# Kernel optimization log

Measured on AMD Instinct MI355X. Metric: run time of the kernel, lower is better.

Reference implementation:

```python
import jax, jax.numpy as jnp
import numpy as np

BN_EPS = 1e-5


def conv(x, w, b=None, stride=1, pad=1):
    out = jax.lax.conv_general_dilated(
        x, w, (stride, stride), [(pad, pad), (pad, pad)],
        dimension_numbers=("NCHW", "OIHW", "NCHW"))
    if b is not None:
        out = out + b[None, :, None, None]
    return out


def bn_relu(x):
    # BatchNorm2d(affine=False) in training mode: per-channel batch stats
    mean = jnp.mean(x, axis=(0, 2, 3), keepdims=True)
    var = jnp.var(x, axis=(0, 2, 3), keepdims=True)
    return jax.nn.relu((x - mean) * jax.lax.rsqrt(var + BN_EPS))


def deform_conv(x, offset, w, b, stride, pad=1):
    # torchvision DeformConv2d semantics, 3x3 kernel, dilation=1
    B, C, H, W = x.shape
    O = w.shape[0]
    K = 9
    Ho, Wo = offset.shape[2], offset.shape[3]
    off = offset.reshape(B, K, 2, Ho, Wo)  # (dy, dx) per kernel tap
    ky, kx = jnp.meshgrid(jnp.arange(3), jnp.arange(3), indexing="ij")
    ky = ky.reshape(K).astype(x.dtype)
    kx = kx.reshape(K).astype(x.dtype)
    oy = (jnp.arange(Ho) * stride - pad).astype(x.dtype)
    ox = (jnp.arange(Wo) * stride - pad).astype(x.dtype)
    # sampling coords [B,K,Ho,Wo]
    ys = oy[None, None, :, None] + ky[None, :, None, None] + off[:, :, 0]
    xs = ox[None, None, None, :] + kx[None, :, None, None] + off[:, :, 1]
    y0 = jnp.floor(ys)
    x0 = jnp.floor(xs)
    wy1 = ys - y0
    wx1 = xs - x0
    imf = x.reshape(B, C, H * W)

    def gather(iy, ix):
        valid = (iy >= 0) & (iy <= H - 1) & (ix >= 0) & (ix <= W - 1)
        iyc = jnp.clip(iy, 0, H - 1).astype(jnp.int32)
        ixc = jnp.clip(ix, 0, W - 1).astype(jnp.int32)
        lin = iyc * W + ixc  # [B,K,Ho,Wo]
        g = jax.vmap(lambda im, li: im[:, li])(imf, lin)  # [B,C,K,Ho,Wo]
        return g * valid[:, None].astype(x.dtype)

    sampled = (gather(y0, x0) * ((1 - wy1) * (1 - wx1))[:, None]
               + gather(y0, x0 + 1) * ((1 - wy1) * wx1)[:, None]
               + gather(y0 + 1, x0) * (wy1 * (1 - wx1))[:, None]
               + gather(y0 + 1, x0 + 1) * (wy1 * wx1)[:, None])
    out = jnp.einsum("ock,bckhw->bohw", w.reshape(O, C, K), sampled)
    return out + b[None, :, None, None]


def avgpool4(x):
    B, C, H, W = x.shape
    return x.reshape(B, C, H // 4, 4, W // 4, 4).mean(axis=(3, 5))


def setup_inputs() -> dict:
    key = jax.random.key(0)
    ks = jax.random.split(key, 20)
    n = jax.random.normal
    s = 0.05
    return {
        "x": n(ks[0], (8, 3, 640, 640), jnp.float32),
        "w_off1": n(ks[1], (18, 3, 3, 3), jnp.float32) * s,
        "b_off1": jnp.zeros((18,), jnp.float32),
        "w_d1": n(ks[2], (64, 3, 3, 3), jnp.float32) * s,
        "b_d1": jnp.zeros((64,), jnp.float32),
        "w_skip": n(ks[3], (64, 3, 1, 1), jnp.float32) * s,
        "b_skip": jnp.zeros((64,), jnp.float32),
        "w_bl1": n(ks[4], (64, 64, 3, 3), jnp.float32) * s,
        "w_bl2": n(ks[5], (64, 64, 3, 3), jnp.float32) * s,
        "w_off2": n(ks[6], (18, 64, 3, 3), jnp.float32) * s,
        "b_off2": jnp.zeros((18,), jnp.float32),
        "w_d2": n(ks[7], (64, 64, 3, 3), jnp.float32) * s,
        "b_d2": jnp.zeros((64,), jnp.float32),
        "w_off3": n(ks[8], (18, 64, 3, 3), jnp.float32) * s,
        "b_off3": jnp.zeros((18,), jnp.float32),
        "w_d3": n(ks[9], (256, 64, 3, 3), jnp.float32) * s,
        "b_d3": jnp.zeros((256,), jnp.float32),
    }


def reference(x, w_off1, b_off1, w_d1, b_d1, w_skip, b_skip, w_bl1, w_bl2,
              w_off2, b_off2, w_d2, b_d2, w_off3, b_off3, w_d3, b_d3):
    offset1 = conv(x, w_off1, b_off1, stride=4)
    d1 = deform_conv(x, offset1, w_d1, b_d1, stride=4)
    skip = conv(avgpool4(x), w_skip, b_skip, stride=1, pad=0)
    f = bn_relu(conv(d1 + skip, w_bl1))
    feat_1_4 = bn_relu(conv(f, w_bl2))
    offset2 = conv(feat_1_4, w_off2, b_off2, stride=2)
    feat_1_8 = deform_conv(feat_1_4, offset2, w_d2, b_d2, stride=2)
    offset3 = conv(feat_1_8, w_off3, b_off3, stride=2)
    feat_1_16 = deform_conv(feat_1_8, offset3, w_d3, b_d3, stride=2)
    return (feat_1_4, feat_1_8, feat_1_16)
```

## Files before the change

kernel.cpp:

```cpp
#include <hip/hip_runtime.h>
#include <hip/hip_bf16.h>
#include <math.h>

#define TPB 256

typedef __attribute__((ext_vector_type(8))) short bf16x8_t;
typedef __attribute__((ext_vector_type(4))) float f32x4_t;
typedef __attribute__((ext_vector_type(4))) int i32x4_t;
typedef __attribute__((ext_vector_type(4))) unsigned short u16x4_t;

static __device__ __forceinline__ float bf16_to_f(unsigned short s) {
    union { unsigned u; float f; } cv;
    cv.u = ((unsigned)s) << 16;
    return cv.f;
}
static __device__ __forceinline__ short f_to_bf16(float v) {
    __hip_bfloat16 h = __float2bfloat16(v);
    return *(short*)&h;
}

__global__ void repack_frag_kernel(const float* __restrict__ w,
                                   short* __restrict__ wtf,
                                   int Oreal, int NFRAG)
{
    int idx = blockIdx.x * TPB + threadIdx.x;
    int total = 18 * NFRAG * 64 * 8;
    if (idx >= total) return;
    int j    = idx & 7;
    int lane = (idx >> 3) & 63;
    int t    = idx >> 9;
    int ocf  = t % NFRAG;
    int kc   = t / NFRAG;
    int oc   = ocf * 16 + (lane & 15);
    int tap  = kc >> 1;
    int ic   = (kc & 1) * 32 + (lane >> 4) * 8 + j;
    float v = 0.f;
    if (oc < Oreal)
        v = w[((size_t)(oc * 64 + ic)) * 9 + tap];
    wtf[idx] = f_to_bf16(v);
}

template <int NORM>
__global__ __launch_bounds__(256, 2) void conv3x3_mfma_kernel(
    const short* __restrict__ xh,
    const short* __restrict__ wt,
    short* __restrict__ outh,
    float* __restrict__ stats,
    const float* __restrict__ stats_in,
    float invN,
    const float* __restrict__ zp)
{
    __shared__ short tile[2816 * 8];
    __shared__ float sstat[128];
    __shared__ float sm[64], sr[64];
    const int H = 160, W = 160, HW = 25600;
    int blk = blockIdx.x;
    int b  = blk / 100;
    int r  = blk % 100;
    int y0 = (r / 10) * 16;
    int x0 = (r % 10) * 16;
    const int tid = threadIdx.x;
    const short* inb = xh + (size_t)b * HW * 64;

    if (tid < 128) sstat[tid] = 0.f;
    if (NORM) {
        if (tid < 64) {
            float s = 0.f, s2 = 0.f;
#pragma unroll
            for (int k = 0; k < 8; ++k) {
                s  += stats_in[k * 128 + tid];
                s2 += stats_in[k * 128 + 64 + tid];
            }
            float mean = s * invN;
            float var  = s2 * invN - mean * mean;
            sm[tid] = mean;
            sr[tid] = rsqrtf(var + 1e-5f);
        }
        __syncthreads();
    }

#pragma unroll
    for (int it = 0; it < 11; ++it) {
        int item = it * 256 + tid;
        int c8  = item & 7;
        int pix = item >> 3;
        int row = pix / 18;
        int col = pix - row * 18;
        int y = y0 + row - 1;
        int x = x0 + col - 1;
        bool ok = (pix < 324) & (y >= 0) & (y < H) & (x >= 0) & (x < W);
        int cs = c8 ^ (col & 7);
        const short* src = ok
            ? &inb[((size_t)y * W + x) * 64 + (cs << 3)]
            : (const short*)zp;
        bf16x8_t v = *(const bf16x8_t*)src;
        if (NORM) {
            int cs8 = cs << 3;
            bf16x8_t o;
#pragma unroll
            for (int j = 0; j < 8; ++j) {
                float f = (bf16_to_f((unsigned short)v[j]) - sm[cs8 + j]) * sr[cs8 + j];
                f = f > 0.f ? f : 0.f;
                o[j] = ok ? f_to_bf16(f) : (short)0;
            }
            v = o;
        }
        *(bf16x8_t*)&tile[item * 8] = v;
    }
    __syncthreads();

    const int wv  = tid >> 6;
    const int l   = tid & 63;
    const int l15 = l & 15;
    const int lg  = l >> 4;

    f32x4_t acc[4][4];
#pragma unroll
    for (int i = 0; i < 4; ++i)
#pragma unroll
        for (int j = 0; j < 4; ++j)
            acc[i][j] = (f32x4_t){0.f, 0.f, 0.f, 0.f};

    bf16x8_t bfp[2][4], afp[2][4];
#pragma unroll
    for (int nf = 0; nf < 4; ++nf)
        bfp[0][nf] = *(const bf16x8_t*)(wt + (((size_t)(0 * 4 + nf)) * 64 + l) * 8);
    {
        int colr = l15;
        int chunk = lg ^ (colr & 7);
#pragma unroll
        for (int mf = 0; mf < 4; ++mf)
            afp[0][mf] = *(const bf16x8_t*)&tile[((wv * 4 + mf) * 18 + colr) * 64 + chunk * 8];
    }
#pragma unroll
    for (int kc = 0; kc < 18; ++kc) {
        const int cur = kc & 1, nxt = cur ^ 1;
        if (kc + 1 < 18) {
            int kn = kc + 1;
#pragma unroll
            for (int nf = 0; nf < 4; ++nf)
                bfp[nxt][nf] = *(const bf16x8_t*)(wt + (((size_t)(kn * 4 + nf)) * 64 + l) * 8);
            int tap = kn >> 1;
            int dy = tap / 3, dx = tap % 3;
            int colr = l15 + dx;
            int chunk = (((kn & 1) << 2) + lg) ^ (colr & 7);
#pragma unroll
            for (int mf = 0; mf < 4; ++mf)
                afp[nxt][mf] = *(const bf16x8_t*)&tile[((wv * 4 + mf + dy) * 18 + colr) * 64 + chunk * 8];
        }
#pragma unroll
        for (int mf = 0; mf < 4; ++mf)
#pragma unroll
            for (int nf = 0; nf < 4; ++nf)
                acc[mf][nf] = __builtin_amdgcn_mfma_f32_16x16x32_bf16(
                    afp[cur][mf], bfp[cur][nf], acc[mf][nf], 0, 0, 0);
    }

    __syncthreads();
#pragma unroll
    for (int mf = 0; mf < 4; ++mf) {
        int py = wv * 4 + mf;
#pragma unroll
        for (int nf = 0; nf < 4; ++nf) {
            int oc = nf * 16 + l15;
#pragma unroll
            for (int k = 0; k < 4; ++k)
                tile[((py * 16) + lg * 4 + k) * 64 + oc] = f_to_bf16(acc[mf][nf][k]);
        }
    }
    __syncthreads();
    short* outb = outh + (size_t)b * HW * 64;
#pragma unroll
    for (int j = 0; j < 8; ++j) {
        int item = j * 256 + tid;
        int c8  = item & 7;
        int pix = item >> 3;
        int py  = pix >> 4, px = pix & 15;
        *(bf16x8_t*)&outb[((size_t)(y0 + py) * W + x0 + px) * 64 + c8 * 8] =
            *(bf16x8_t*)&tile[pix * 64 + c8 * 8];
    }

#pragma unroll
    for (int nf = 0; nf < 4; ++nf) {
        float s = 0.f, s2 = 0.f;
#pragma unroll
        for (int mf = 0; mf < 4; ++mf)
#pragma unroll
            for (int k = 0; k < 4; ++k) {
                float v = acc[mf][nf][k];
                s += v; s2 += v * v;
            }
        s  += __shfl_xor(s, 16, 64);  s  += __shfl_xor(s, 32, 64);
        s2 += __shfl_xor(s2, 16, 64); s2 += __shfl_xor(s2, 32, 64);
        if (lg == 0) {
            int oc = nf * 16 + l15;
            atomicAdd(&sstat[oc], s);
            atomicAdd(&sstat[64 + oc], s2);
        }
    }
    __syncthreads();
    float* st = stats + (size_t)(blockIdx.x & 7) * 128;
    if (tid < 128) atomicAdd(&st[tid], sstat[tid]);
}

__global__ void nchw_to_nhwc_bf16_kernel(const float* __restrict__ in,
                                         short* __restrict__ out, int HW)
{
    __shared__ short tile[64][66];
    int nchunks = HW >> 6;
    int b  = blockIdx.x / nchunks;
    int p0 = (blockIdx.x % nchunks) << 6;
    int tid = threadIdx.x;
#pragma unroll
    for (int rep = 0; rep < 16; ++rep) {
        int item = rep * 256 + tid;
        int c = item >> 6, p = item & 63;
        tile[p][c] = f_to_bf16(in[((size_t)b * 64 + c) * HW + p0 + p]);
    }
    __syncthreads();
#pragma unroll
    for (int rep = 0; rep < 16; ++rep) {
        int item = rep * 256 + tid;
        int p = item >> 6, c = item & 63;
        out[((size_t)b * HW + p0 + p) * 64 + c] = tile[p][c];
    }
}

__global__ void bn_apply_dual_kernel(const short* __restrict__ in,
                                     const float* __restrict__ stats,
                                     float* __restrict__ out,
                                     short* __restrict__ outh,
                                     int HW, float invN)
{
    __shared__ float ftile[64][65];
    __shared__ float sm[64], sr[64];
    int nchunks = HW >> 6;
    int b  = blockIdx.x / nchunks;
    int p0 = (blockIdx.x % nchunks) << 6;
    int tid = threadIdx.x;
    if (tid < 64) {
        float s = 0.f, s2 = 0.f;
#pragma unroll
        for (int k = 0; k < 8; ++k) {
            s  += stats[k * 128 + tid];
            s2 += stats[k * 128 + 64 + tid];
        }
        float mean = s * invN;
        float var  = s2 * invN - mean * mean;
        sm[tid] = mean;
        sr[tid] = rsqrtf(var + 1e-5f);
    }
    __syncthreads();
#pragma unroll
    for (int it = 0; it < 2; ++it) {
        int item = it * 256 + tid;
        int p = item >> 3, c0 = (item & 7) * 8;
        size_t gi = ((size_t)(b * HW + p0 + p)) * 64 + c0;
        bf16x8_t v = *(const bf16x8_t*)&in[gi];
        bf16x8_t o;
#pragma unroll
        for (int j = 0; j < 8; ++j) {
            float f = (bf16_to_f((unsigned short)v[j]) - sm[c0 + j]) * sr[c0 + j];
            f = f > 0.f ? f : 0.f;
            ftile[p][c0 + j] = f;
            o[j] = f_to_bf16(f);
        }
        *(bf16x8_t*)&outh[gi] = o;
    }
    __syncthreads();
#pragma unroll
    for (int rep = 0; rep < 16; ++rep) {
        int item = rep * 256 + tid;
        int c = item >> 6, p = item & 63;
        out[((size_t)b * 64 + c) * HW + p0 + p] = ftile[p][c];
    }
}

__global__ void x_to_nhwc4_kernel(const float* __restrict__ in,
                                  float* __restrict__ out)
{
    int idx = blockIdx.x * TPB + threadIdx.x;
    const int HW = 640 * 640;
    if (idx >= 8 * HW) return;
    int b = idx / HW, p = idx % HW;
    f32x4_t v;
    v[0] = in[((size_t)b * 3 + 0) * HW + p];
    v[1] = in[((size_t)b * 3 + 1) * HW + p];
    v[2] = in[((size_t)b * 3 + 2) * HW + p];
    v[3] = 0.f;
    *(f32x4_t*)&out[(size_t)idx * 4] = v;
}

__global__ __launch_bounds__(256, 1) void offconv_mfma_kernel(
    const short* __restrict__ xh,
    const short* __restrict__ wt,
    const float* __restrict__ bias,
    float* __restrict__ out,
    int H, int W, int Ho, int Wo)
{
    const int HW = Ho * Wo;
    const int tid = threadIdx.x;
    const int wv = tid >> 6, l = tid & 63;
    const int l15 = l & 15, lg = l >> 4;
    const int pix0 = blockIdx.x * 64 + wv * 16;
    const int b = pix0 / HW;
    const int r0 = pix0 - b * HW;

    int rp = r0 + l15;
    int ho = rp / Wo, wo = rp % Wo;
    const short* xb = xh + (size_t)b * H * W * 64;

    f32x4_t acc[2];
    acc[0] = (f32x4_t){0.f, 0.f, 0.f, 0.f};
    acc[1] = (f32x4_t){0.f, 0.f, 0.f, 0.f};

#pragma unroll 2
    for (int kc = 0; kc < 18; ++kc) {
        int tap = kc >> 1;
        int iy = ho * 2 - 1 + tap / 3;
        int ix = wo * 2 - 1 + tap % 3;
        bf16x8_t af = {};
        if (iy >= 0 && iy < H && ix >= 0 && ix < W)
            af = *(const bf16x8_t*)&xb[((size_t)iy * W + ix) * 64
                                       + (kc & 1) * 32 + lg * 8];
#pragma unroll
        for (int nf = 0; nf < 2; ++nf) {
            bf16x8_t bf = *(const bf16x8_t*)(wt + (((size_t)(kc * 2 + nf)) * 64 + l) * 8);
            acc[nf] = __builtin_amdgcn_mfma_f32_16x16x32_bf16(af, bf, acc[nf], 0, 0, 0);
        }
    }

#pragma unroll
    for (int nf = 0; nf < 2; ++nf) {
        int oc = nf * 16 + l15;
        if (oc < 18) {
            float bv = bias[oc];
            f32x4_t v = acc[nf];
            v[0] += bv; v[1] += bv; v[2] += bv; v[3] += bv;
            *(f32x4_t*)&out[((size_t)(b * 18 + oc)) * HW + r0 + lg * 4] = v;
        }
    }
}

__global__ __launch_bounds__(256, 1) void deform1_kernel(
    const float* __restrict__ x4,
    const float* __restrict__ wof,
    const float* __restrict__ bof,
    const float* __restrict__ w,
    const float* __restrict__ bias,
    const float* __restrict__ pool,
    const float* __restrict__ wsk,
    const float* __restrict__ bsk,
    short* __restrict__ outh)
{
    const int H = 640, W = 640, Ho = 160, Wo = 160, HW = 25600;
    constexpr int P = 32;
    __shared__ float xtap[P * 9][4];
    __shared__ float swof[486];
    __shared__ float sbof[18];
    __shared__ float off1[P][18];
    __shared__ float samp[P][28];
    __shared__ int   sidx[P * 9][4];
    __shared__ float swt[P * 9][4];
    const int tid = threadIdx.x;
    const int pix0 = blockIdx.x * P;
    const int b = pix0 / HW;
    const int r0 = pix0 - b * HW;
    const float* xb = x4 + (size_t)b * H * W * 4;

    for (int item = tid; item < P * 9; item += TPB) {
        int p = item / 9, tap = item % 9;
        int r = r0 + p, ho = r / Wo, wo = r % Wo;
        int iy = ho * 4 - 1 + tap / 3;
        int ix = wo * 4 - 1 + tap % 3;
        f32x4_t s = (f32x4_t){0.f, 0.f, 0.f, 0.f};
        if (iy >= 0 && iy < H && ix >= 0 && ix < W)
            s = *(const f32x4_t*)&xb[((size_t)iy * W + ix) * 4];
        *(f32x4_t*)xtap[item] = s;
    }
    for (int item = tid; item < 486; item += TPB) swof[item] = wof[item];
    if (tid < 18) sbof[tid] = bof[tid];
    __syncthreads();

    for (int item = tid; item < P * 18; item += TPB) {
        int p = item / 18, o = item % 18;
        float acc = sbof[o];
#pragma unroll
        for (int tap = 0; tap < 9; ++tap) {
            const float* xt = xtap[p * 9 + tap];
#pragma unroll
            for (int c = 0; c < 3; ++c)
                acc += xt[c] * swof[(o * 3 + c) * 9 + tap];
        }
        off1[p][o] = acc;
    }
    __syncthreads();

    for (int item = tid; item < P * 9; item += TPB) {
        int p = item / 9, tap = item % 9;
        int r = r0 + p, ho = r / Wo, wo = r % Wo;
        float dy = off1[p][2 * tap];
        float dx = off1[p][2 * tap + 1];
        float ys = (float)(ho * 4 - 1 + tap / 3) + dy;
        float xs = (float)(wo * 4 - 1 + tap % 3) + dx;
        float y0f = floorf(ys), x0f = floorf(xs);
        float fy = ys - y0f, fx = xs - x0f;
        int y0 = (int)y0f, x0 = (int)x0f;
        float wts[4] = {(1.f - fy) * (1.f - fx), (1.f - fy) * fx,
                        fy * (1.f - fx),          fy * fx};
#pragma unroll
        for (int j = 0; j < 4; ++j) {
            int iy = y0 + (j >> 1), ix = x0 + (j & 1);
            bool v = (iy >= 0) && (iy < H) && (ix >= 0) && (ix < W);
            sidx[item][j] = v ? (iy * W + ix) : 0;
            swt[item][j]  = v ? wts[j] : 0.f;
        }
    }
    __syncthreads();

    for (int item = tid; item < P * 9; item += TPB) {
        int p = item / 9, tap = item % 9;
        i32x4_t id4 = *(const i32x4_t*)sidx[item];
        f32x4_t w4  = *(const f32x4_t*)swt[item];
        f32x4_t a0 = *(const f32x4_t*)&xb[(size_t)(unsigned)id4[0] * 4];
        f32x4_t a1 = *(const f32x4_t*)&xb[(size_t)(unsigned)id4[1] * 4];
        f32x4_t a2 = *(const f32x4_t*)&xb[(size_t)(unsigned)id4[2] * 4];
        f32x4_t a3 = *(const f32x4_t*)&xb[(size_t)(unsigned)id4[3] * 4];
        samp[p][0 * 9 + tap] = w4[0]*a0[0] + w4[1]*a1[0] + w4[2]*a2[0] + w4[3]*a3[0];
        samp[p][1 * 9 + tap] = w4[0]*a0[1] + w4[1]*a1[1] + w4[2]*a2[1] + w4[3]*a3[1];
        samp[p][2 * 9 + tap] = w4[0]*a0[2] + w4[1]*a1[2] + w4[2]*a2[2] + w4[3]*a3[2];
    }
    __syncthreads();

    int g = tid >> 6;
    int o = tid & 63;
    float acc[8];
#pragma unroll
    for (int pi = 0; pi < 8; ++pi) acc[pi] = bias[o] + bsk[o];
#pragma unroll
    for (int c = 0; c < 3; ++c)
#pragma unroll
        for (int k = 0; k < 9; ++k) {
            float wv = w[((size_t)(o * 3 + c)) * 9 + k];
#pragma unroll
            for (int pi = 0; pi < 8; ++pi)
                acc[pi] += wv * samp[g * 8 + pi][c * 9 + k];
        }
#pragma unroll
    for (int pi = 0; pi < 8; ++pi) {
        int r = r0 + g * 8 + pi;
        float sv = wsk[o * 3 + 0] * pool[(size_t)(b * 3 + 0) * HW + r]
                 + wsk[o * 3 + 1] * pool[(size_t)(b * 3 + 1) * HW + r]
                 + wsk[o * 3 + 2] * pool[(size_t)(b * 3 + 2) * HW + r];
        outh[((size_t)(b * HW + r)) * 64 + o] = f_to_bf16(acc[pi] + sv);
    }
}

template <int O>
__global__ __launch_bounds__(256, 1) void deform_mfma_kernel(
    const short* __restrict__ xh,
    const float* __restrict__ off,
    const short* __restrict__ wt,
    const float* __restrict__ bias,
    float* __restrict__ out,
    int H, int W, int Ho, int Wo, int stride)
{
    constexpr int NF = O / 64;
    constexpr int NFRAG = O / 16;
    constexpr int P  = 32;
    __shared__ alignas(16) short samp[P * 576];
    __shared__ int   sidx[P * 9][4];
    __shared__ float swt[P * 9][4];

    const int tid = threadIdx.x;
    const int HW = Ho * Wo;
    const int pix0 = blockIdx.x * P;
    const int b = pix0 / HW;
    const int r0 = pix0 - b * HW;

    for (int item = tid; item < P * 9; item += TPB) {
        int p = item / 9, tap = item % 9;
        int r = r0 + p, ho = r / Wo, wo = r % Wo;
        float dy = off[((size_t)(b * 18 + 2 * tap) * Ho + ho) * Wo + wo];
        float dx = off[((size_t)(b * 18 + 2 * tap + 1) * Ho + ho) * Wo + wo];
        float ys = (float)(ho * stride - 1 + tap / 3) + dy;
        float xs = (float)(wo * stride - 1 + tap % 3) + dx;
        float y0f = floorf(ys), x0f = floorf(xs);
        float fy = ys - y0f, fx = xs - x0f;
        int y0 = (int)y0f, x0 = (int)x0f;
        float wts[4] = {(1.f - fy) * (1.f - fx), (1.f - fy) * fx,
                        fy * (1.f - fx),          fy * fx};
#pragma unroll
        for (int j = 0; j < 4; ++j) {
            int iy = y0 + (j >> 1), ix = x0 + (j & 1);
            bool v = (iy >= 0) && (iy < H) && (ix >= 0) && (ix < W);
            sidx[item][j] = v ? (iy * W + ix) : 0;
            swt[item][j]  = v ? wts[j] : 0.f;
        }
    }
    __syncthreads();

    {
        const int grp = tid >> 4;
        const int ic  = (tid & 15) * 4;
        const short* xb = xh + (size_t)b * H * W * 64;
#pragma unroll 3
        for (int i = 0; i < 18; ++i) {
            int e = grp * 18 + i;
            int p = e / 9, tap = e % 9;
            i32x4_t id4 = *(const i32x4_t*)sidx[e];
            f32x4_t w4  = *(const f32x4_t*)swt[e];
            u16x4_t u0 = *(const u16x4_t*)&xb[(size_t)(unsigned)id4[0] * 64 + ic];
            u16x4_t u1 = *(const u16x4_t*)&xb[(size_t)(unsigned)id4[1] * 64 + ic];
            u16x4_t u2 = *(const u16x4_t*)&xb[(size_t)(unsigned)id4[2] * 64 + ic];
            u16x4_t u3 = *(const u16x4_t*)&xb[(size_t)(unsigned)id4[3] * 64 + ic];
            float v0 = w4[0]*bf16_to_f(u0[0]) + w4[1]*bf16_to_f(u1[0])
                     + w4[2]*bf16_to_f(u2[0]) + w4[3]*bf16_to_f(u3[0]);
            float v1 = w4[0]*bf16_to_f(u0[1]) + w4[1]*bf16_to_f(u1[1])
                     + w4[2]*bf16_to_f(u2[1]) + w4[3]*bf16_to_f(u3[1]);
            float v2 = w4[0]*bf16_to_f(u0[2]) + w4[1]*bf16_to_f(u1[2])
                     + w4[2]*bf16_to_f(u2[2]) + w4[3]*bf16_to_f(u3[2]);
            float v3 = w4[0]*bf16_to_f(u0[3]) + w4[1]*bf16_to_f(u1[3])
                     + w4[2]*bf16_to_f(u2[3]) + w4[3]*bf16_to_f(u3[3]);
            int sw = (tap * 8 + ((ic >> 3) ^ (p & 7))) * 8 + (ic & 7);
            short* dst = &samp[p * 576 + sw];
            dst[0] = f_to_bf16(v0);
            dst[1] = f_to_bf16(v1);
            dst[2] = f_to_bf16(v2);
            dst[3] = f_to_bf16(v3);
        }
    }
    __syncthreads();

    const int wv = tid >> 6;
    const int l  = tid & 63;
    const int l15 = l & 15, lg = l >> 4;
    f32x4_t acc[2][NF];
#pragma unroll
    for (int mf = 0; mf < 2; ++mf)
#pragma unroll
        for (int nf = 0; nf < NF; ++nf)
            acc[mf][nf] = (f32x4_t){0.f, 0.f, 0.f, 0.f};

#pragma unroll 2
    for (int kc = 0; kc < 18; ++kc) {
        int tap = kc >> 1;
        int low = (((kc & 1) << 2) | lg) ^ (l15 & 7);
        bf16x8_t af0 = *(const bf16x8_t*)&samp[l15 * 576 + (tap * 8 + low) * 8];
        bf16x8_t af1 = *(const bf16x8_t*)&samp[(l15 + 16) * 576 + (tap * 8 + low) * 8];
#pragma unroll
        for (int nf = 0; nf < NF; ++nf) {
            int ocf = wv * NF + nf;
            bf16x8_t bf = *(const bf16x8_t*)(wt + (((size_t)(kc * NFRAG + ocf)) * 64 + l) * 8);
            acc[0][nf] = __builtin_amdgcn_mfma_f32_16x16x32_bf16(af0, bf, acc[0][nf], 0, 0, 0);
            acc[1][nf] = __builtin_amdgcn_mfma_f32_16x16x32_bf16(af1, bf, acc[1][nf], 0, 0, 0);
        }
    }

#pragma unroll
    for (int mf = 0; mf < 2; ++mf)
#pragma unroll
        for (int nf = 0; nf < NF; ++nf) {
            int oc = (wv * NF + nf) * 16 + l15;
            float bv = bias[oc];
            f32x4_t v = acc[mf][nf];
            v[0] += bv; v[1] += bv; v[2] += bv; v[3] += bv;
            *(f32x4_t*)&out[((size_t)(b * O + oc)) * HW + r0 + mf * 16 + lg * 4] = v;
        }
}

__global__ void avgpool4_kernel(const float* __restrict__ in,
                                float* __restrict__ out,
                                int BC, int Ho, int Wo, int H, int W)
{
    int idx = blockIdx.x * TPB + threadIdx.x;
    int total = BC * Ho * Wo;
    if (idx >= total) return;
    int wo = idx % Wo;
    int t = idx / Wo;
    int ho = t % Ho;
    int bc = t / Ho;
    const float* xp = in + (size_t)bc * H * W + (ho * 4) * W + wo * 4;
    float s = 0.f;
#pragma unroll
    for (int i = 0; i < 4; ++i)
#pragma unroll
        for (int j = 0; j < 4; ++j)
            s += xp[i * W + j];
    out[idx] = s * (1.0f / 16.0f);
}

__global__ void zero_stats_kernel(float* __restrict__ stats)
{
    int i = threadIdx.x;
#pragma unroll
    for (int k = 0; k < 8; ++k) stats[k * 256 + i] = 0.f;
    stats[2048 + i] = 0.f;
    stats[2048 + 256 + i] = 0.f;
}

extern "C" void kernel_launch(void* const* d_in, const int* in_sizes, int n_in,
                              void* d_out, int out_size, void* d_ws, size_t ws_size,
                              hipStream_t stream)
{
    const float* x      = (const float*)d_in[0];
    const float* w_off1 = (const float*)d_in[1];
    const float* b_off1 = (const float*)d_in[2];
    const float* w_d1   = (const float*)d_in[3];
    const float* b_d1   = (const float*)d_in[4];
    const float* w_skip = (const float*)d_in[5];
    const float* b_skip = (const float*)d_in[6];
    const float* w_bl1  = (const float*)d_in[7];
    const float* w_bl2  = (const float*)d_in[8];
    const float* w_off2 = (const float*)d_in[9];
    const float* b_off2 = (const float*)d_in[10];
    const float* w_d2   = (const float*)d_in[11];
    const float* b_d2   = (const float*)d_in[12];
    const float* w_off3 = (const float*)d_in[13];
    const float* b_off3 = (const float*)d_in[14];
    const float* w_d3   = (const float*)d_in[15];
    const float* b_d3   = (const float*)d_in[16];

    const int B = 8;
    float* A     = (float*)d_ws;
    float* bufB  = A + 3686400;
    float* bufC  = bufB + 13107200;

    short* hB   = (short*)bufB;
    short* hC   = (short*)bufC;
    float* pool = bufB + 8000000;

    short* wt1    = (short*)(A + 1000000);
    short* wt2    = wt1 + 18 * 4 * 512;
    short* wtd2   = (short*)(A + 1500000);
    short* wtd3   = (short*)(A + 1550000);
    short* wtoff2 = (short*)(A + 1700000);
    short* wtoff3 = (short*)(A + 1712000);
    float* stats1 = A + 1800000;
    float* stats2 = stats1 + 1024;
    float* zpage  = stats1 + 2048;

    float* out0 = (float*)d_out;
    float* out1 = out0 + 13107200;
    float* out2 = out1 + 3276800;

    const float invN = 1.0f / (B * 25600);

    x_to_nhwc4_kernel<<<(8 * 409600 + TPB - 1) / TPB, TPB, 0, stream>>>(x, bufC);

    avgpool4_kernel<<<(B * 3 * 25600 + TPB - 1) / TPB, TPB, 0, stream>>>(
        x, pool, B * 3, 160, 160, 640, 640);

    repack_frag_kernel<<<(18 * 4 * 512 + TPB - 1) / TPB, TPB, 0, stream>>>(w_bl1, wt1, 64, 4);
    repack_frag_kernel<<<(18 * 4 * 512 + TPB - 1) / TPB, TPB, 0, stream>>>(w_bl2, wt2, 64, 4);
    repack_frag_kernel<<<(18 * 4 * 512 + TPB - 1) / TPB, TPB, 0, stream>>>(w_d2, wtd2, 64, 4);
    repack_frag_kernel<<<(18 * 16 * 512 + TPB - 1) / TPB, TPB, 0, stream>>>(w_d3, wtd3, 256, 16);
    repack_frag_kernel<<<(18 * 2 * 512 + TPB - 1) / TPB, TPB, 0, stream>>>(w_off2, wtoff2, 18, 2);
    repack_frag_kernel<<<(18 * 2 * 512 + TPB - 1) / TPB, TPB, 0, stream>>>(w_off3, wtoff3, 18, 2);
    zero_stats_kernel<<<1, 256, 0, stream>>>(stats1);

    deform1_kernel<<<8 * 25600 / 32, TPB, 0, stream>>>(
        bufC, w_off1, b_off1, w_d1, b_d1, pool, w_skip, b_skip, hB);

    conv3x3_mfma_kernel<0><<<800, TPB, 0, stream>>>(
        hB, wt1, hC, stats1, nullptr, invN, zpage);

    conv3x3_mfma_kernel<1><<<800, TPB, 0, stream>>>(
        hC, wt2, hB, stats2, stats1, invN, zpage);

    bn_apply_dual_kernel<<<8 * 400, TPB, 0, stream>>>(
        hB, stats2, out0, hC, 25600, invN);

    offconv_mfma_kernel<<<8 * 6400 / 64, TPB, 0, stream>>>(
        hC, wtoff2, b_off2, A, 160, 160, 80, 80);

    deform_mfma_kernel<64><<<8 * 6400 / 32, TPB, 0, stream>>>(
        hC, A, wtd2, b_d2, out1, 160, 160, 80, 80, 2);

    nchw_to_nhwc_bf16_kernel<<<8 * (6400 / 64), TPB, 0, stream>>>(out1, hB, 6400);

    offconv_mfma_kernel<<<8 * 1600 / 64, TPB, 0, stream>>>(
        hB, wtoff3, b_off3, A, 80, 80, 40, 40);

    deform_mfma_kernel<256><<<8 * 1600 / 32, TPB, 0, stream>>>(
        hB, A, wtd3, b_d3, out2, 80, 80, 40, 40, 2);
}
```

Measured before the change: 245.4 us.

## Use MFMA for first deformable conv projection with LDS-staged coalesced stores

Replaces the scalar FMA loop in deform1_kernel, which projects the 27 sampled values per pixel onto 64 output channels, with one bf16 MFMA 16x16x32 per wave per 16-pixel fragment. The weights are pre-packed into fragment layout by a new repack kernel. The pooled skip input is staged in LDS, and outputs are staged through an LDS tile so each pixel's 64 channels are written with 16-byte stores. This removes redundant weight and pool global reads and strided 2-byte stores, at the cost of rounding the sampled values to bf16 and adding extra barriers.

```diff
diff --git a/kernel.cpp b/kernel.cpp
--- a/kernel.cpp
+++ b/kernel.cpp
@@ -37,6 +37,21 @@
     float v = 0.f;
     if (oc < Oreal)
         v = w[((size_t)(oc * 64 + ic)) * 9 + tap];
+    wtf[idx] = f_to_bf16(v);
+}
+
+__global__ void repack_d1_kernel(const float* __restrict__ w,
+                                 short* __restrict__ wtf)
+{
+    int idx = blockIdx.x * TPB + threadIdx.x;
+    if (idx >= 2048) return;
+    int j    = idx & 7;
+    int lane = (idx >> 3) & 63;
+    int ocf  = idx >> 9;
+    int oc   = ocf * 16 + (lane & 15);
+    int k    = (lane >> 4) * 8 + j;
+    float v = 0.f;
+    if (k < 27) v = w[(size_t)oc * 27 + k];
     wtf[idx] = f_to_bf16(v);
 }
 
@@ -346,7 +361,7 @@
     const float* __restrict__ x4,
     const float* __restrict__ wof,
     const float* __restrict__ bof,
-    const float* __restrict__ w,
+    const short* __restrict__ wtd1,
     const float* __restrict__ bias,
     const float* __restrict__ pool,
     const float* __restrict__ wsk,
@@ -358,8 +373,9 @@
     __shared__ float xtap[P * 9][4];
     __shared__ float swof[486];
     __shared__ float sbof[18];
+    __shared__ float spool[3][P];
     __shared__ float off1[P][18];
-    __shared__ float samp[P][28];
+    __shared__ alignas(16) short sampb[P][40];
     __shared__ int   sidx[P * 9][4];
     __shared__ float swt[P * 9][4];
     const int tid = threadIdx.x;
@@ -377,6 +393,11 @@
         if (iy >= 0 && iy < H && ix >= 0 && ix < W)
             s = *(const f32x4_t*)&xb[((size_t)iy * W + ix) * 4];
         *(f32x4_t*)xtap[item] = s;
+    }
+    for (int i = tid; i < P * 40; i += TPB) ((short*)sampb)[i] = 0;
+    for (int i = tid; i < 96; i += TPB) {
+        int c = i >> 5, p = i & 31;
+        spool[c][p] = pool[((size_t)(b * 3 + c)) * HW + r0 + p];
     }
     for (int item = tid; item < 486; item += TPB) swof[item] = wof[item];
     if (tid < 18) sbof[tid] = bof[tid];
@@ -426,33 +447,45 @@
         f32x4_t a1 = *(const f32x4_t*)&xb[(size_t)(unsigned)id4[1] * 4];
         f32x4_t a2 = *(const f32x4_t*)&xb[(size_t)(unsigned)id4[2] * 4];
         f32x4_t a3 = *(const f32x4_t*)&xb[(size_t)(unsigned)id4[3] * 4];
-        samp[p][0 * 9 + tap] = w4[0]*a0[0] + w4[1]*a1[0] + w4[2]*a2[0] + w4[3]*a3[0];
-        samp[p][1 * 9 + tap] = w4[0]*a0[1] + w4[1]*a1[1] + w4[2]*a2[1] + w4[3]*a3[1];
-        samp[p][2 * 9 + tap] = w4[0]*a0[2] + w4[1]*a1[2] + w4[2]*a2[2] + w4[3]*a3[2];
-    }
-    __syncthreads();
-
-    int g = tid >> 6;
-    int o = tid & 63;
-    float acc[8];
-#pragma unroll
-    for (int pi = 0; pi < 8; ++pi) acc[pi] = bias[o] + bsk[o];
-#pragma unroll
-    for (int c = 0; c < 3; ++c)
-#pragma unroll
-        for (int k = 0; k < 9; ++k) {
-            float wv = w[((size_t)(o * 3 + c)) * 9 + k];
-#pragma unroll
-            for (int pi = 0; pi < 8; ++pi)
-                acc[pi] += wv * samp[g * 8 + pi][c * 9 + k];
-        }
-#pragma unroll
-    for (int pi = 0; pi < 8; ++pi) {
-        int r = r0 + g * 8 + pi;
-        float sv = wsk[o * 3 + 0] * pool[(size_t)(b * 3 + 0) * HW + r]
-                 + wsk[o * 3 + 1] * pool[(size_t)(b * 3 + 1) * HW + r]
-                 + wsk[o * 3 + 2] * pool[(size_t)(b * 3 + 2) * HW + r];
-        outh[((size_t)(b * HW + r)) * 64 + o] = f_to_bf16(acc[pi] + sv);
+        sampb[p][0 * 9 + tap] = f_to_bf16(
+            w4[0]*a0[0] + w4[1]*a1[0] + w4[2]*a2[0] + w4[3]*a3[0]);
+        sampb[p][1 * 9 + tap] = f_to_bf16(
+            w4[0]*a0[1] + w4[1]*a1[1] + w4[2]*a2[1] + w4[3]*a3[1]);
+        sampb[p][2 * 9 + tap] = f_to_bf16(
+            w4[0]*a0[2] + w4[1]*a1[2] + w4[2]*a2[2] + w4[3]*a3[2]);
+    }
+    __syncthreads();
+
+    const int wv = tid >> 6;
+    const int l  = tid & 63;
+    const int l15 = l & 15, lg = l >> 4;
+    bf16x8_t bf  = *(const bf16x8_t*)(wtd1 + (((size_t)wv * 64 + l)) * 8);
+    bf16x8_t af0 = *(const bf16x8_t*)&sampb[l15][lg * 8];
+    bf16x8_t af1 = *(const bf16x8_t*)&sampb[l15 + 16][lg * 8];
+    f32x4_t z = (f32x4_t){0.f, 0.f, 0.f, 0.f};
+    f32x4_t acc0 = __builtin_amdgcn_mfma_f32_16x16x32_bf16(af0, bf, z, 0, 0, 0);
+    f32x4_t acc1 = __builtin_amdgcn_mfma_f32_16x16x32_bf16(af1, bf, z, 0, 0, 0);
+
+    int oc = wv * 16 + l15;
+    float bb = bias[oc] + bsk[oc];
+    float w0 = wsk[oc * 3 + 0], w1 = wsk[oc * 3 + 1], w2 = wsk[oc * 3 + 2];
+    short* otile = (short*)xtap;
+    __syncthreads();
+#pragma unroll
+    for (int mf = 0; mf < 2; ++mf) {
+        f32x4_t a = mf ? acc1 : acc0;
+#pragma unroll
+        for (int k = 0; k < 4; ++k) {
+            int px = mf * 16 + lg * 4 + k;
+            float sv = w0 * spool[0][px] + w1 * spool[1][px] + w2 * spool[2][px];
+            otile[px * 64 + oc] = f_to_bf16(a[k] + bb + sv);
+        }
+    }
+    __syncthreads();
+    {
+        int c8 = tid & 7, px = tid >> 3;
+        *(bf16x8_t*)&outh[((size_t)(b * HW + r0 + px)) * 64 + c8 * 8] =
+            *(bf16x8_t*)&otile[px * 64 + c8 * 8];
     }
 }
 
@@ -636,6 +669,7 @@
     short* wtd3   = (short*)(A + 1550000);
     short* wtoff2 = (short*)(A + 1700000);
     short* wtoff3 = (short*)(A + 1712000);
+    short* wtd1   = (short*)(A + 1750000);
     float* stats1 = A + 1800000;
     float* stats2 = stats1 + 1024;
     float* zpage  = stats1 + 2048;
@@ -657,10 +691,11 @@
     repack_frag_kernel<<<(18 * 16 * 512 + TPB - 1) / TPB, TPB, 0, stream>>>(w_d3, wtd3, 256, 16);
     repack_frag_kernel<<<(18 * 2 * 512 + TPB - 1) / TPB, TPB, 0, stream>>>(w_off2, wtoff2, 18, 2);
     repack_frag_kernel<<<(18 * 2 * 512 + TPB - 1) / TPB, TPB, 0, stream>>>(w_off3, wtoff3, 18, 2);
+    repack_d1_kernel<<<8, TPB, 0, stream>>>(w_d1, wtd1);
     zero_stats_kernel<<<1, 256, 0, stream>>>(stats1);
 
     deform1_kernel<<<8 * 25600 / 32, TPB, 0, stream>>>(
-        bufC, w_off1, b_off1, w_d1, b_d1, pool, w_skip, b_skip, hB);
+        bufC, w_off1, b_off1, wtd1, b_d1, pool, w_skip, b_skip, hB);
 
     conv3x3_mfma_kernel<0><<<800, TPB, 0, stream>>>(
         hB, wt1, hC, stats1, nullptr, invN, zpage);
```

Measured after the change: 238.0 us. 1.03x faster.
